# Kernel tuning notes

Hardware: AMD Instinct MI355X
Metric: run time of the kernel (lower is better)

The kernel has to match this reference:

```python
import jax, jax.numpy as jnp
import numpy as np

EPS = 1e-10
BETA_SCALE = 1.0
TEMP = 0.5


def setup_inputs() -> dict:
    key = jax.random.key(0)
    ks = jax.random.split(key, 8)
    D = 128
    return {
        "root_mu_min": jax.random.normal(ks[0], (1, 64, D), dtype=jnp.float32),
        "root_mu_max": jax.random.normal(ks[1], (1, 64, D), dtype=jnp.float32),
        "root_beta_min_raw": jax.random.normal(ks[2], (1, 64, D), dtype=jnp.float32),
        "root_beta_max_raw": jax.random.normal(ks[3], (1, 64, D), dtype=jnp.float32),
        "adj_logits0": jax.random.normal(ks[4], (512, 64), dtype=jnp.float32),
        "adj_logits1": jax.random.normal(ks[5], (2048, 512), dtype=jnp.float32),
        "u0": jax.random.uniform(ks[6], (1, 512, 64), dtype=jnp.float32),
        "u1": jax.random.uniform(ks[7], (1, 2048, 512), dtype=jnp.float32),
    }


def _gumbel_sigmoid_hard(logits, u):
    # gumbel noise from externally supplied uniforms, straight-through hard threshold
    g = -jnp.log(-jnp.log(u + EPS) + EPS)
    y_soft = jax.nn.sigmoid((logits + g) / TEMP)
    y_hard = (y_soft > 0.5).astype(y_soft.dtype)
    return y_hard - jax.lax.stop_gradient(y_soft) + y_soft


def _weighted_intersection(mu_min, mu_max, beta_min, beta_max, w):
    # w: (1, C, P); parent boxes: (1, P, D)
    wsum = jnp.sum(w, axis=2)[..., None] + EPS                      # (1, C, 1)
    b_min = jnp.einsum('bcp,bpd->bcd', w, beta_min) / wsum           # (1, C, D)
    b_max = jnp.einsum('bcp,bpd->bcd', w, beta_max) / wsum           # (1, C, D)
    logw = jnp.log(w + EPS)[..., None]                               # (1, C, P, 1)
    arg_min = logw + mu_min[:, None, :, :] / b_min[:, :, None, :]    # (1, C, P, D)
    mu_min_i = b_min * jax.nn.logsumexp(arg_min, axis=2)             # (1, C, D)
    arg_max = logw - mu_max[:, None, :, :] / b_max[:, :, None, :]    # (1, C, P, D)
    mu_max_i = -b_max * jax.nn.logsumexp(arg_max, axis=2)            # (1, C, D)
    return mu_min_i, mu_max_i, b_min, b_max


def reference(root_mu_min, root_mu_max, root_beta_min_raw, root_beta_max_raw,
              adj_logits0, adj_logits1, u0, u1):
    beta_min = jax.nn.sigmoid(root_beta_min_raw) * BETA_SCALE + 1e-6
    beta_max = jax.nn.sigmoid(root_beta_max_raw) * BETA_SCALE + 1e-6
    level = (root_mu_min, root_mu_max, beta_min, beta_max)
    outs = list(level)
    for logits, u in ((adj_logits0, u0), (adj_logits1, u1)):
        w = _gumbel_sigmoid_hard(logits[None], u)  # (1, C, P)
        level = _weighted_intersection(*level, w)
        outs.extend(level)
    return tuple(outs)
```

## Files before the change

kernel.cpp:

```cpp
#include <hip/hip_runtime.h>
#include <cmath>

#define DD 128
#define LOG2E 1.4426950408889634f

__device__ __forceinline__ float sigm(float x) { return 1.0f / (1.0f + __expf(-x)); }

__device__ __forceinline__ unsigned fenc(float f) {
    unsigned b = __float_as_uint(f);
    return (b & 0x80000000u) ? ~b : (b | 0x80000000u);
}
__device__ __forceinline__ float fdec(unsigned e) {
    return (e & 0x80000000u) ? __uint_as_float(e ^ 0x80000000u) : __uint_as_float(~e);
}

__global__ __launch_bounds__(512)
void k_root0(const float* __restrict__ mu_min, const float* __restrict__ mu_max,
             const float* __restrict__ braw_min, const float* __restrict__ braw_max,
             float* __restrict__ out,
             float2* __restrict__ mu2_0, float2* __restrict__ bb2_0,
             unsigned* __restrict__ e_min0, unsigned* __restrict__ e_neg0) {
    __shared__ float r1[4][DD], r2[4][DD];
    const int i = blockIdx.x * 512 + threadIdx.x;
    const int rg = threadIdx.x >> 7, d = threadIdx.x & (DD - 1);
    float mn = mu_min[i], mx = mu_max[i];
    float bm = sigm(braw_min[i]) + 1e-6f;
    float bx = sigm(braw_max[i]) + 1e-6f;
    out[i] = mn; out[8192 + i] = mx; out[16384 + i] = bm; out[24576 + i] = bx;
    mu2_0[i] = make_float2(mn, mx);
    bb2_0[i] = make_float2(bm, bx);
    r1[rg][d] = mn; r2[rg][d] = -mx;
    __syncthreads();
    if (threadIdx.x < DD) {
        float a = fmaxf(fmaxf(r1[0][d], r1[1][d]), fmaxf(r1[2][d], r1[3][d]));
        float b = fmaxf(fmaxf(r2[0][d], r2[1][d]), fmaxf(r2[2][d], r2[3][d]));
        atomicMax(e_min0 + d, fenc(a));
        atomicMax(e_neg0 + d, fenc(b));
        if (blockIdx.x == 0) {
            mu2_0[64 * DD + d] = make_float2(-1e38f, 1e38f);
            bb2_0[64 * DD + d] = make_float2(0.0f, 0.0f);
        }
    }
}

template<int P, int RPB>
__global__ __launch_bounds__(512)
void k_packprep(const float* __restrict__ mu_min, const float* __restrict__ mu_max,
                const float* __restrict__ b_min, const float* __restrict__ b_max,
                float2* __restrict__ mu2, float2* __restrict__ bb2,
                unsigned* __restrict__ e_min, unsigned* __restrict__ e_neg) {
    __shared__ float s1[4][DD], s2[4][DD];
    const int d = threadIdx.x & (DD - 1);
    const int rg = threadIdx.x >> 7;
    const int r0 = blockIdx.x * RPB;
    float m1 = -INFINITY, m2 = -INFINITY;
    for (int r = rg; r < RPB; r += 4) {
        int i = (r0 + r) * DD + d;
        float a = mu_min[i], b = mu_max[i];
        mu2[i] = make_float2(a, b);
        bb2[i] = make_float2(b_min[i], b_max[i]);
        m1 = fmaxf(m1, a);
        m2 = fmaxf(m2, -b);
    }
    s1[rg][d] = m1; s2[rg][d] = m2;
    __syncthreads();
    if (threadIdx.x < DD) {
        float a = fmaxf(fmaxf(s1[0][d], s1[1][d]), fmaxf(s1[2][d], s1[3][d]));
        float b = fmaxf(fmaxf(s2[0][d], s2[1][d]), fmaxf(s2[2][d], s2[3][d]));
        atomicMax(e_min + d, fenc(a));
        atomicMax(e_neg + d, fenc(b));
        if (blockIdx.x == 0) {
            mu2[P * DD + d] = make_float2(-1e38f, 1e38f);
            bb2[P * DD + d] = make_float2(0.0f, 0.0f);
        }
    }
}

template<int P>
__global__ __launch_bounds__(256, 4)
void k_levelw(const float* __restrict__ logits, const float* __restrict__ u,
              const float2* __restrict__ bb2, const float2* __restrict__ mu2,
              const unsigned* __restrict__ e_min, const unsigned* __restrict__ e_neg,
              float* __restrict__ o_mu_min, float* __restrict__ o_mu_max,
              float* __restrict__ o_b_min, float* __restrict__ o_b_max) {
    __shared__ __align__(16) int plist[2][P];
    __shared__ float4 red[2][2][64];
    const int tid = threadIdx.x;
    const int w = tid >> 6;
    const int lane = tid & 63;
    const int j = w >> 1, h = w & 1;
    const int c = blockIdx.x * 2 + j;
    int* pl = plist[j];

    int base = 0;
    #pragma unroll
    for (int it = 0; it < P / 64; ++it) {
        int p = it * 64 + lane;
        int idx = c * P + p;
        float uu = u[idx] + 1e-10f;
        float g = -__logf(-__logf(uu) + 1e-10f);
        bool pres = (logits[idx] + g) > 0.0f;
        unsigned long long m = __ballot(pres);
        if (pres) {
            int pos = __popcll(m & ((1ull << lane) - 1));
            pl[base + pos] = p << 10;
        }
        base += (int)__popcll(m);
    }
    const int n = base;
    int npad = (n + 15) & ~15;
    if (npad == 0) npad = 16;
    if (lane < npad - n) pl[n + lane] = P << 10;

    const unsigned lb = (unsigned)(lane << 4);
    const char* bbc = (const char*)bb2;
    const char* muc = (const char*)mu2;
    const int Th = npad >> 4;

    float dmn0 = 0.f, dmx0 = 0.f, dmn1 = 0.f, dmx1 = 0.f;
    {
        float4 q[8];
        int k = h * 8;
        {
            int4 A = *(const int4*)(pl + k);
            int4 B = *(const int4*)(pl + k + 4);
            q[0] = *(const float4*)(bbc + ((unsigned)A.x + lb));
            q[1] = *(const float4*)(bbc + ((unsigned)A.y + lb));
            q[2] = *(const float4*)(bbc + ((unsigned)A.z + lb));
            q[3] = *(const float4*)(bbc + ((unsigned)A.w + lb));
            q[4] = *(const float4*)(bbc + ((unsigned)B.x + lb));
            q[5] = *(const float4*)(bbc + ((unsigned)B.y + lb));
            q[6] = *(const float4*)(bbc + ((unsigned)B.z + lb));
            q[7] = *(const float4*)(bbc + ((unsigned)B.w + lb));
        }
        for (int t = 1; t < Th; ++t) {
            k += 16;
            int4 A = *(const int4*)(pl + k);
            int4 B = *(const int4*)(pl + k + 4);
            float4 qn[8];
            qn[0] = *(const float4*)(bbc + ((unsigned)A.x + lb));
            qn[1] = *(const float4*)(bbc + ((unsigned)A.y + lb));
            qn[2] = *(const float4*)(bbc + ((unsigned)A.z + lb));
            qn[3] = *(const float4*)(bbc + ((unsigned)A.w + lb));
            qn[4] = *(const float4*)(bbc + ((unsigned)B.x + lb));
            qn[5] = *(const float4*)(bbc + ((unsigned)B.y + lb));
            qn[6] = *(const float4*)(bbc + ((unsigned)B.z + lb));
            qn[7] = *(const float4*)(bbc + ((unsigned)B.w + lb));
            dmn0 += (q[0].x + q[1].x) + (q[2].x + q[3].x) + (q[4].x + q[5].x) + (q[6].x + q[7].x);
            dmx0 += (q[0].y + q[1].y) + (q[2].y + q[3].y) + (q[4].y + q[5].y) + (q[6].y + q[7].y);
            dmn1 += (q[0].z + q[1].z) + (q[2].z + q[3].z) + (q[4].z + q[5].z) + (q[6].z + q[7].z);
            dmx1 += (q[0].w + q[1].w) + (q[2].w + q[3].w) + (q[4].w + q[5].w) + (q[6].w + q[7].w);
            #pragma unroll
            for (int z = 0; z < 8; ++z) q[z] = qn[z];
        }
        dmn0 += (q[0].x + q[1].x) + (q[2].x + q[3].x) + (q[4].x + q[5].x) + (q[6].x + q[7].x);
        dmx0 += (q[0].y + q[1].y) + (q[2].y + q[3].y) + (q[4].y + q[5].y) + (q[6].y + q[7].y);
        dmn1 += (q[0].z + q[1].z) + (q[2].z + q[3].z) + (q[4].z + q[5].z) + (q[6].z + q[7].z);
        dmx1 += (q[0].w + q[1].w) + (q[2].w + q[3].w) + (q[4].w + q[5].w) + (q[6].w + q[7].w);
    }
    red[j][h][lane] = make_float4(dmn0, dmx0, dmn1, dmx1);
    __syncthreads();

    float4 pb0 = red[j][0][lane];
    float4 pb1 = red[j][1][lane];
    const float wsv = (float)n + 1e-10f;
    const float bmin0 = (pb0.x + pb1.x) / wsv;
    const float bmax0 = (pb0.y + pb1.y) / wsv;
    const float bmin1 = (pb0.z + pb1.z) / wsv;
    const float bmax1 = (pb0.w + pb1.w) / wsv;
    const float rmin0 = 1.0f / fmaxf(bmin0, 1e-30f);
    const float rmin1 = 1.0f / fmaxf(bmin1, 1e-30f);
    const float nrmax0 = -1.0f / fmaxf(bmax0, 1e-30f);
    const float nrmax1 = -1.0f / fmaxf(bmax1, 1e-30f);
    uint2 em = *(const uint2*)(e_min + 2 * lane);
    uint2 en = *(const uint2*)(e_neg + 2 * lane);
    const float Mm0 = fdec(em.x), Mm1 = fdec(em.y);
    const float Mg0 = fdec(en.x), Mg1 = fdec(en.y);
    const float rm20 = rmin0 * LOG2E, rm21 = rmin1 * LOG2E;
    const float nx20 = nrmax0 * LOG2E, nx21 = nrmax1 * LOG2E;
    const float nM10 = -rm20 * Mm0, nM11 = -rm21 * Mm1;
    const float nM20 = nx20 * Mg0, nM21 = nx21 * Mg1;
    __syncthreads();

    float s10 = 0.f, s20 = 0.f, s11 = 0.f, s21 = 0.f;
    {
        float4 q[8];
        int k = h * 8;
        {
            int4 A = *(const int4*)(pl + k);
            int4 B = *(const int4*)(pl + k + 4);
            q[0] = *(const float4*)(muc + ((unsigned)A.x + lb));
            q[1] = *(const float4*)(muc + ((unsigned)A.y + lb));
            q[2] = *(const float4*)(muc + ((unsigned)A.z + lb));
            q[3] = *(const float4*)(muc + ((unsigned)A.w + lb));
            q[4] = *(const float4*)(muc + ((unsigned)B.x + lb));
            q[5] = *(const float4*)(muc + ((unsigned)B.y + lb));
            q[6] = *(const float4*)(muc + ((unsigned)B.z + lb));
            q[7] = *(const float4*)(muc + ((unsigned)B.w + lb));
        }
        for (int t = 1; t < Th; ++t) {
            k += 16;
            int4 A = *(const int4*)(pl + k);
            int4 B = *(const int4*)(pl + k + 4);
            float4 qn[8];
            qn[0] = *(const float4*)(muc + ((unsigned)A.x + lb));
            qn[1] = *(const float4*)(muc + ((unsigned)A.y + lb));
            qn[2] = *(const float4*)(muc + ((unsigned)A.z + lb));
            qn[3] = *(const float4*)(muc + ((unsigned)A.w + lb));
            qn[4] = *(const float4*)(muc + ((unsigned)B.x + lb));
            qn[5] = *(const float4*)(muc + ((unsigned)B.y + lb));
            qn[6] = *(const float4*)(muc + ((unsigned)B.z + lb));
            qn[7] = *(const float4*)(muc + ((unsigned)B.w + lb));
            #pragma unroll
            for (int z = 0; z < 8; ++z) {
                s10 += __builtin_amdgcn_exp2f(fmaf(q[z].x, rm20, nM10));
                s20 += __builtin_amdgcn_exp2f(fmaf(q[z].y, nx20, nM20));
                s11 += __builtin_amdgcn_exp2f(fmaf(q[z].z, rm21, nM11));
                s21 += __builtin_amdgcn_exp2f(fmaf(q[z].w, nx21, nM21));
            }
            #pragma unroll
            for (int z = 0; z < 8; ++z) q[z] = qn[z];
        }
        #pragma unroll
        for (int z = 0; z < 8; ++z) {
            s10 += __builtin_amdgcn_exp2f(fmaf(q[z].x, rm20, nM10));
            s20 += __builtin_amdgcn_exp2f(fmaf(q[z].y, nx20, nM20));
            s11 += __builtin_amdgcn_exp2f(fmaf(q[z].z, rm21, nM11));
            s21 += __builtin_amdgcn_exp2f(fmaf(q[z].w, nx21, nM21));
        }
    }
    red[j][h][lane] = make_float4(s10, s20, s11, s21);
    __syncthreads();

    if (h == 0) {
        float4 pc0 = red[j][0][lane];
        float4 pc1 = red[j][1][lane];
        const float S10 = fmaxf(pc0.x + pc1.x, 1e-35f);
        const float S20 = fmaxf(pc0.y + pc1.y, 1e-35f);
        const float S11 = fmaxf(pc0.z + pc1.z, 1e-35f);
        const float S21 = fmaxf(pc0.w + pc1.w, 1e-35f);
        const int idx = c * DD + 2 * lane;
        float v10 = bmin0 * fmaf(rmin0, Mm0, __logf(S10));
        float v11 = bmin1 * fmaf(rmin1, Mm1, __logf(S11));
        float v20 = -bmax0 * fmaf(-nrmax0, Mg0, __logf(S20));
        float v21 = -bmax1 * fmaf(-nrmax1, Mg1, __logf(S21));
        *(float2*)(o_mu_min + idx) = make_float2(v10, v11);
        *(float2*)(o_mu_max + idx) = make_float2(v20, v21);
        *(float2*)(o_b_min + idx)  = make_float2(bmin0, bmin1);
        *(float2*)(o_b_max + idx)  = make_float2(bmax0, bmax1);
    }
}

extern "C" void kernel_launch(void* const* d_in, const int* in_sizes, int n_in,
                              void* d_out, int out_size, void* d_ws, size_t ws_size,
                              hipStream_t stream) {
    const float* mu_min0  = (const float*)d_in[0];
    const float* mu_max0  = (const float*)d_in[1];
    const float* braw_min = (const float*)d_in[2];
    const float* braw_max = (const float*)d_in[3];
    const float* adj0     = (const float*)d_in[4];
    const float* adj1     = (const float*)d_in[5];
    const float* u0       = (const float*)d_in[6];
    const float* u1       = (const float*)d_in[7];
    float* out = (float*)d_out;
    float* ws = (float*)d_ws;

    unsigned* cm_enc  = (unsigned*)ws;
    unsigned* cm0_min = cm_enc;
    unsigned* cm0_neg = cm_enc + 128;
    unsigned* cm1_min = cm_enc + 256;
    unsigned* cm1_neg = cm_enc + 384;
    float2* mu2_0 = (float2*)(ws + 512);
    float2* bb2_0 = mu2_0 + 65 * DD;
    float2* mu2_1 = bb2_0 + 65 * DD;
    float2* bb2_1 = mu2_1 + 513 * DD;


    hipMemsetAsync(cm_enc, 0, 512 * sizeof(unsigned), stream);

    k_root0<<<dim3(16), dim3(512), 0, stream>>>(
        mu_min0, mu_max0, braw_min, braw_max, out, mu2_0, bb2_0, cm0_min, cm0_neg);

    k_levelw<64><<<dim3(256), dim3(256), 0, stream>>>(
        adj0, u0, bb2_0, mu2_0, cm0_min, cm0_neg,
        out + 32768, out + 98304, out + 163840, out + 229376);

    k_packprep<512, 8><<<dim3(64), dim3(512), 0, stream>>>(
        out + 32768, out + 98304, out + 163840, out + 229376, mu2_1, bb2_1, cm1_min, cm1_neg);

    k_levelw<512><<<dim3(1024), dim3(256), 0, stream>>>(
        adj1, u1, bb2_1, mu2_1, cm1_min, cm1_neg,
        out + 294912, out + 557056, out + 819200, out + 1081344);
}
```

Baseline: 132.1 us.

## Replace sparse gather level-1 kernel with dense 4-child tiled weighted kernel

```diff
diff --git a/kernel.cpp b/kernel.cpp
--- a/kernel.cpp
+++ b/kernel.cpp
@@ -118,45 +118,22 @@
     const int Th = npad >> 4;
 
     float dmn0 = 0.f, dmx0 = 0.f, dmn1 = 0.f, dmx1 = 0.f;
-    {
-        float4 q[8];
-        int k = h * 8;
-        {
-            int4 A = *(const int4*)(pl + k);
-            int4 B = *(const int4*)(pl + k + 4);
-            q[0] = *(const float4*)(bbc + ((unsigned)A.x + lb));
-            q[1] = *(const float4*)(bbc + ((unsigned)A.y + lb));
-            q[2] = *(const float4*)(bbc + ((unsigned)A.z + lb));
-            q[3] = *(const float4*)(bbc + ((unsigned)A.w + lb));
-            q[4] = *(const float4*)(bbc + ((unsigned)B.x + lb));
-            q[5] = *(const float4*)(bbc + ((unsigned)B.y + lb));
-            q[6] = *(const float4*)(bbc + ((unsigned)B.z + lb));
-            q[7] = *(const float4*)(bbc + ((unsigned)B.w + lb));
-        }
-        for (int t = 1; t < Th; ++t) {
-            k += 16;
-            int4 A = *(const int4*)(pl + k);
-            int4 B = *(const int4*)(pl + k + 4);
-            float4 qn[8];
-            qn[0] = *(const float4*)(bbc + ((unsigned)A.x + lb));
-            qn[1] = *(const float4*)(bbc + ((unsigned)A.y + lb));
-            qn[2] = *(const float4*)(bbc + ((unsigned)A.z + lb));
-            qn[3] = *(const float4*)(bbc + ((unsigned)A.w + lb));
-            qn[4] = *(const float4*)(bbc + ((unsigned)B.x + lb));
-            qn[5] = *(const float4*)(bbc + ((unsigned)B.y + lb));
-            qn[6] = *(const float4*)(bbc + ((unsigned)B.z + lb));
-            qn[7] = *(const float4*)(bbc + ((unsigned)B.w + lb));
-            dmn0 += (q[0].x + q[1].x) + (q[2].x + q[3].x) + (q[4].x + q[5].x) + (q[6].x + q[7].x);
-            dmx0 += (q[0].y + q[1].y) + (q[2].y + q[3].y) + (q[4].y + q[5].y) + (q[6].y + q[7].y);
-            dmn1 += (q[0].z + q[1].z) + (q[2].z + q[3].z) + (q[4].z + q[5].z) + (q[6].z + q[7].z);
-            dmx1 += (q[0].w + q[1].w) + (q[2].w + q[3].w) + (q[4].w + q[5].w) + (q[6].w + q[7].w);
-            #pragma unroll
-            for (int z = 0; z < 8; ++z) q[z] = qn[z];
-        }
-        dmn0 += (q[0].x + q[1].x) + (q[2].x + q[3].x) + (q[4].x + q[5].x) + (q[6].x + q[7].x);
-        dmx0 += (q[0].y + q[1].y) + (q[2].y + q[3].y) + (q[4].y + q[5].y) + (q[6].y + q[7].y);
-        dmn1 += (q[0].z + q[1].z) + (q[2].z + q[3].z) + (q[4].z + q[5].z) + (q[6].z + q[7].z);
-        dmx1 += (q[0].w + q[1].w) + (q[2].w + q[3].w) + (q[4].w + q[5].w) + (q[6].w + q[7].w);
+    for (int t = 0; t < Th; ++t) {
+        int k = h * 8 + t * 16;
+        int4 A = *(const int4*)(pl + k);
+        int4 B = *(const int4*)(pl + k + 4);
+        float4 q0 = *(const float4*)(bbc + ((unsigned)A.x + lb));
+        float4 q1 = *(const float4*)(bbc + ((unsigned)A.y + lb));
+        float4 q2 = *(const float4*)(bbc + ((unsigned)A.z + lb));
+        float4 q3 = *(const float4*)(bbc + ((unsigned)A.w + lb));
+        float4 q4 = *(const float4*)(bbc + ((unsigned)B.x + lb));
+        float4 q5 = *(const float4*)(bbc + ((unsigned)B.y + lb));
+        float4 q6 = *(const float4*)(bbc + ((unsigned)B.z + lb));
+        float4 q7 = *(const float4*)(bbc + ((unsigned)B.w + lb));
+        dmn0 += (q0.x + q1.x) + (q2.x + q3.x) + (q4.x + q5.x) + (q6.x + q7.x);
+        dmx0 += (q0.y + q1.y) + (q2.y + q3.y) + (q4.y + q5.y) + (q6.y + q7.y);
+        dmn1 += (q0.z + q1.z) + (q2.z + q3.z) + (q4.z + q5.z) + (q6.z + q7.z);
+        dmx1 += (q0.w + q1.w) + (q2.w + q3.w) + (q4.w + q5.w) + (q6.w + q7.w);
     }
     red[j][h][lane] = make_float4(dmn0, dmx0, dmn1, dmx1);
     __syncthreads();
@@ -183,51 +160,50 @@
     __syncthreads();
 
     float s10 = 0.f, s20 = 0.f, s11 = 0.f, s21 = 0.f;
-    {
-        float4 q[8];
-        int k = h * 8;
-        {
-            int4 A = *(const int4*)(pl + k);
-            int4 B = *(const int4*)(pl + k + 4);
-            q[0] = *(const float4*)(muc + ((unsigned)A.x + lb));
-            q[1] = *(const float4*)(muc + ((unsigned)A.y + lb));
-            q[2] = *(const float4*)(muc + ((unsigned)A.z + lb));
-            q[3] = *(const float4*)(muc + ((unsigned)A.w + lb));
-            q[4] = *(const float4*)(muc + ((unsigned)B.x + lb));
-            q[5] = *(const float4*)(muc + ((unsigned)B.y + lb));
-            q[6] = *(const float4*)(muc + ((unsigned)B.z + lb));
-            q[7] = *(const float4*)(muc + ((unsigned)B.w + lb));
-        }
-        for (int t = 1; t < Th; ++t) {
-            k += 16;
-            int4 A = *(const int4*)(pl + k);
-            int4 B = *(const int4*)(pl + k + 4);
-            float4 qn[8];
-            qn[0] = *(const float4*)(muc + ((unsigned)A.x + lb));
-            qn[1] = *(const float4*)(muc + ((unsigned)A.y + lb));
-            qn[2] = *(const float4*)(muc + ((unsigned)A.z + lb));
-            qn[3] = *(const float4*)(muc + ((unsigned)A.w + lb));
-            qn[4] = *(const float4*)(muc + ((unsigned)B.x + lb));
-            qn[5] = *(const float4*)(muc + ((unsigned)B.y + lb));
-            qn[6] = *(const float4*)(muc + ((unsigned)B.z + lb));
-            qn[7] = *(const float4*)(muc + ((unsigned)B.w + lb));
-            #pragma unroll
-            for (int z = 0; z < 8; ++z) {
-                s10 += __builtin_amdgcn_exp2f(fmaf(q[z].x, rm20, nM10));
-                s20 += __builtin_amdgcn_exp2f(fmaf(q[z].y, nx20, nM20));
-                s11 += __builtin_amdgcn_exp2f(fmaf(q[z].z, rm21, nM11));
-                s21 += __builtin_amdgcn_exp2f(fmaf(q[z].w, nx21, nM21));
-            }
-            #pragma unroll
-            for (int z = 0; z < 8; ++z) q[z] = qn[z];
-        }
-        #pragma unroll
-        for (int z = 0; z < 8; ++z) {
-            s10 += __builtin_amdgcn_exp2f(fmaf(q[z].x, rm20, nM10));
-            s20 += __builtin_amdgcn_exp2f(fmaf(q[z].y, nx20, nM20));
-            s11 += __builtin_amdgcn_exp2f(fmaf(q[z].z, rm21, nM11));
-            s21 += __builtin_amdgcn_exp2f(fmaf(q[z].w, nx21, nM21));
-        }
+    for (int t = 0; t < Th; ++t) {
+        int k = h * 8 + t * 16;
+        int4 A = *(const int4*)(pl + k);
+        int4 B = *(const int4*)(pl + k + 4);
+        float4 q0 = *(const float4*)(muc + ((unsigned)A.x + lb));
+        float4 q1 = *(const float4*)(muc + ((unsigned)A.y + lb));
+        float4 q2 = *(const float4*)(muc + ((unsigned)A.z + lb));
+        float4 q3 = *(const float4*)(muc + ((unsigned)A.w + lb));
+        float4 q4 = *(const float4*)(muc + ((unsigned)B.x + lb));
+        float4 q5 = *(const float4*)(muc + ((unsigned)B.y + lb));
+        float4 q6 = *(const float4*)(muc + ((unsigned)B.z + lb));
+        float4 q7 = *(const float4*)(muc + ((unsigned)B.w + lb));
+        s10 += __builtin_amdgcn_exp2f(fmaf(q0.x, rm20, nM10));
+        s20 += __builtin_amdgcn_exp2f(fmaf(q0.y, nx20, nM20));
+        s11 += __builtin_amdgcn_exp2f(fmaf(q0.z, rm21, nM11));
+        s21 += __builtin_amdgcn_exp2f(fmaf(q0.w, nx21, nM21));
+        s10 += __builtin_amdgcn_exp2f(fmaf(q1.x, rm20, nM10));
+        s20 += __builtin_amdgcn_exp2f(fmaf(q1.y, nx20, nM20));
+        s11 += __builtin_amdgcn_exp2f(fmaf(q1.z, rm21, nM11));
+        s21 += __builtin_amdgcn_exp2f(fmaf(q1.w, nx21, nM21));
+        s10 += __builtin_amdgcn_exp2f(fmaf(q2.x, rm20, nM10));
+        s20 += __builtin_amdgcn_exp2f(fmaf(q2.y, nx20, nM20));
+        s11 += __builtin_amdgcn_exp2f(fmaf(q2.z, rm21, nM11));
+        s21 += __builtin_amdgcn_exp2f(fmaf(q2.w, nx21, nM21));
+        s10 += __builtin_amdgcn_exp2f(fmaf(q3.x, rm20, nM10));
+        s20 += __builtin_amdgcn_exp2f(fmaf(q3.y, nx20, nM20));
+        s11 += __builtin_amdgcn_exp2f(fmaf(q3.z, rm21, nM11));
+        s21 += __builtin_amdgcn_exp2f(fmaf(q3.w, nx21, nM21));
+        s10 += __builtin_amdgcn_exp2f(fmaf(q4.x, rm20, nM10));
+        s20 += __builtin_amdgcn_exp2f(fmaf(q4.y, nx20, nM20));
+        s11 += __builtin_amdgcn_exp2f(fmaf(q4.z, rm21, nM11));
+        s21 += __builtin_amdgcn_exp2f(fmaf(q4.w, nx21, nM21));
+        s10 += __builtin_amdgcn_exp2f(fmaf(q5.x, rm20, nM10));
+        s20 += __builtin_amdgcn_exp2f(fmaf(q5.y, nx20, nM20));
+        s11 += __builtin_amdgcn_exp2f(fmaf(q5.z, rm21, nM11));
+        s21 += __builtin_amdgcn_exp2f(fmaf(q5.w, nx21, nM21));
+        s10 += __builtin_amdgcn_exp2f(fmaf(q6.x, rm20, nM10));
+        s20 += __builtin_amdgcn_exp2f(fmaf(q6.y, nx20, nM20));
+        s11 += __builtin_amdgcn_exp2f(fmaf(q6.z, rm21, nM11));
+        s21 += __builtin_amdgcn_exp2f(fmaf(q6.w, nx21, nM21));
+        s10 += __builtin_amdgcn_exp2f(fmaf(q7.x, rm20, nM10));
+        s20 += __builtin_amdgcn_exp2f(fmaf(q7.y, nx20, nM20));
+        s11 += __builtin_amdgcn_exp2f(fmaf(q7.z, rm21, nM11));
+        s21 += __builtin_amdgcn_exp2f(fmaf(q7.w, nx21, nM21));
     }
     red[j][h][lane] = make_float4(s10, s20, s11, s21);
     __syncthreads();
@@ -251,6 +227,151 @@
     }
 }
 
+__global__ __launch_bounds__(512, 4)
+void k_level2d(const float* __restrict__ logits, const float* __restrict__ u,
+               const float2* __restrict__ bb2, const float2* __restrict__ mu2,
+               const unsigned* __restrict__ e_min, const unsigned* __restrict__ e_neg,
+               float* __restrict__ o_mu_min, float* __restrict__ o_mu_max,
+               float* __restrict__ o_b_min, float* __restrict__ o_b_max) {
+    constexpr int P = 512, TC = 4;
+    __shared__ __align__(16) float wsh[P][TC];
+    __shared__ int npres[TC];
+    __shared__ float4 red[8][TC][64];
+    __shared__ float4 carrA[TC][64], carrB[TC][64];
+    const int tid = threadIdx.x;
+    const int w = tid >> 6;
+    const int lane = tid & 63;
+    const int c0 = blockIdx.x * TC;
+    if (tid < TC) npres[tid] = 0;
+    __syncthreads();
+
+    #pragma unroll
+    for (int it = 0; it < TC; ++it) {
+        int i = it * 512 + tid;
+        int j = i >> 9;
+        int p = i & 511;
+        int idx = (c0 + j) * P + p;
+        float uu = u[idx] + 1e-10f;
+        float g = -__logf(-__logf(uu) + 1e-10f);
+        bool pres = (logits[idx] + g) > 0.0f;
+        wsh[p][j] = pres ? 1.0f : 1e-10f;
+        unsigned long long m = __ballot(pres);
+        if (lane == 0) atomicAdd(&npres[j], (int)__popcll(m));
+    }
+    __syncthreads();
+
+    const unsigned lb = (unsigned)(lane << 4);
+    const char* bbc = (const char*)bb2 + (unsigned)(w * 64) * 1024u + lb;
+    const char* muc = (const char*)mu2 + (unsigned)(w * 64) * 1024u + lb;
+    const int p0 = w * 64;
+
+    float4 accB[TC];
+    #pragma unroll
+    for (int j = 0; j < TC; ++j) accB[j] = make_float4(0.f, 0.f, 0.f, 0.f);
+    for (int z = 0; z < 64; z += 4) {
+        float4 q0 = *(const float4*)(bbc + (unsigned)(z + 0) * 1024u);
+        float4 q1 = *(const float4*)(bbc + (unsigned)(z + 1) * 1024u);
+        float4 q2 = *(const float4*)(bbc + (unsigned)(z + 2) * 1024u);
+        float4 q3 = *(const float4*)(bbc + (unsigned)(z + 3) * 1024u);
+        float4 w0 = *(const float4*)wsh[p0 + z + 0];
+        float4 w1 = *(const float4*)wsh[p0 + z + 1];
+        float4 w2 = *(const float4*)wsh[p0 + z + 2];
+        float4 w3 = *(const float4*)wsh[p0 + z + 3];
+        const float* wf0 = (const float*)&w0;
+        const float* wf1 = (const float*)&w1;
+        const float* wf2 = (const float*)&w2;
+        const float* wf3 = (const float*)&w3;
+        #pragma unroll
+        for (int j = 0; j < TC; ++j) {
+            accB[j].x = fmaf(wf0[j], q0.x, fmaf(wf1[j], q1.x, fmaf(wf2[j], q2.x, fmaf(wf3[j], q3.x, accB[j].x))));
+            accB[j].y = fmaf(wf0[j], q0.y, fmaf(wf1[j], q1.y, fmaf(wf2[j], q2.y, fmaf(wf3[j], q3.y, accB[j].y))));
+            accB[j].z = fmaf(wf0[j], q0.z, fmaf(wf1[j], q1.z, fmaf(wf2[j], q2.z, fmaf(wf3[j], q3.z, accB[j].z))));
+            accB[j].w = fmaf(wf0[j], q0.w, fmaf(wf1[j], q1.w, fmaf(wf2[j], q2.w, fmaf(wf3[j], q3.w, accB[j].w))));
+        }
+    }
+    #pragma unroll
+    for (int j = 0; j < TC; ++j) red[w][j][lane] = accB[j];
+    __syncthreads();
+
+    float bmin0, bmax0, bmin1, bmax1, rmin0, rmin1, nrmax0, nrmax1, Mm0, Mm1, Mg0, Mg1;
+    const int rj = tid >> 6;
+    if (tid < 256) {
+        float4 S = red[0][rj][lane];
+        #pragma unroll
+        for (int ww = 1; ww < 8; ++ww) {
+            float4 t = red[ww][rj][lane];
+            S.x += t.x; S.y += t.y; S.z += t.z; S.w += t.w;
+        }
+        const float wsv = (float)npres[rj] + 1e-10f;
+        bmin0 = S.x / wsv; bmax0 = S.y / wsv; bmin1 = S.z / wsv; bmax1 = S.w / wsv;
+        rmin0 = 1.0f / fmaxf(bmin0, 1e-30f);
+        rmin1 = 1.0f / fmaxf(bmin1, 1e-30f);
+        nrmax0 = -1.0f / fmaxf(bmax0, 1e-30f);
+        nrmax1 = -1.0f / fmaxf(bmax1, 1e-30f);
+        uint2 em = *(const uint2*)(e_min + 2 * lane);
+        uint2 en = *(const uint2*)(e_neg + 2 * lane);
+        Mm0 = fdec(em.x); Mm1 = fdec(em.y);
+        Mg0 = fdec(en.x); Mg1 = fdec(en.y);
+        float rm20 = rmin0 * LOG2E, rm21 = rmin1 * LOG2E;
+        float nx20 = nrmax0 * LOG2E, nx21 = nrmax1 * LOG2E;
+        carrA[rj][lane] = make_float4(rm20, rm21, nx20, nx21);
+        carrB[rj][lane] = make_float4(-rm20 * Mm0, -rm21 * Mm1, nx20 * Mg0, nx21 * Mg1);
+    }
+    __syncthreads();
+
+    float4 cA[TC], cB[TC];
+    #pragma unroll
+    for (int j = 0; j < TC; ++j) { cA[j] = carrA[j][lane]; cB[j] = carrB[j][lane]; }
+
+    float4 accS[TC];
+    #pragma unroll
+    for (int j = 0; j < TC; ++j) accS[j] = make_float4(0.f, 0.f, 0.f, 0.f);
+    for (int z = 0; z < 64; z += 2) {
+        float4 q0 = *(const float4*)(muc + (unsigned)(z + 0) * 1024u);
+        float4 q1 = *(const float4*)(muc + (unsigned)(z + 1) * 1024u);
+        float4 w0 = *(const float4*)wsh[p0 + z + 0];
+        float4 w1 = *(const float4*)wsh[p0 + z + 1];
+        const float* wf0 = (const float*)&w0;
+        const float* wf1 = (const float*)&w1;
+        #pragma unroll
+        for (int j = 0; j < TC; ++j) {
+            accS[j].x = fmaf(wf0[j], __builtin_amdgcn_exp2f(fmaf(q0.x, cA[j].x, cB[j].x)), accS[j].x);
+            accS[j].y = fmaf(wf0[j], __builtin_amdgcn_exp2f(fmaf(q0.y, cA[j].z, cB[j].z)), accS[j].y);
+            accS[j].z = fmaf(wf0[j], __builtin_amdgcn_exp2f(fmaf(q0.z, cA[j].y, cB[j].y)), accS[j].z);
+            accS[j].w = fmaf(wf0[j], __builtin_amdgcn_exp2f(fmaf(q0.w, cA[j].w, cB[j].w)), accS[j].w);
+            accS[j].x = fmaf(wf1[j], __builtin_amdgcn_exp2f(fmaf(q1.x, cA[j].x, cB[j].x)), accS[j].x);
+            accS[j].y = fmaf(wf1[j], __builtin_amdgcn_exp2f(fmaf(q1.y, cA[j].z, cB[j].z)), accS[j].y);
+            accS[j].z = fmaf(wf1[j], __builtin_amdgcn_exp2f(fmaf(q1.z, cA[j].y, cB[j].y)), accS[j].z);
+            accS[j].w = fmaf(wf1[j], __builtin_amdgcn_exp2f(fmaf(q1.w, cA[j].w, cB[j].w)), accS[j].w);
+        }
+    }
+    #pragma unroll
+    for (int j = 0; j < TC; ++j) red[w][j][lane] = accS[j];
+    __syncthreads();
+
+    if (tid < 256) {
+        float4 S = red[0][rj][lane];
+        #pragma unroll
+        for (int ww = 1; ww < 8; ++ww) {
+            float4 t = red[ww][rj][lane];
+            S.x += t.x; S.y += t.y; S.z += t.z; S.w += t.w;
+        }
+        const float S10 = fmaxf(S.x, 1e-35f);
+        const float S20 = fmaxf(S.y, 1e-35f);
+        const float S11 = fmaxf(S.z, 1e-35f);
+        const float S21 = fmaxf(S.w, 1e-35f);
+        const int idx = (c0 + rj) * DD + 2 * lane;
+        float v10 = bmin0 * fmaf(rmin0, Mm0, __logf(S10));
+        float v11 = bmin1 * fmaf(rmin1, Mm1, __logf(S11));
+        float v20 = -bmax0 * fmaf(-nrmax0, Mg0, __logf(S20));
+        float v21 = -bmax1 * fmaf(-nrmax1, Mg1, __logf(S21));
+        *(float2*)(o_mu_min + idx) = make_float2(v10, v11);
+        *(float2*)(o_mu_max + idx) = make_float2(v20, v21);
+        *(float2*)(o_b_min + idx)  = make_float2(bmin0, bmin1);
+        *(float2*)(o_b_max + idx)  = make_float2(bmax0, bmax1);
+    }
+}
+
 extern "C" void kernel_launch(void* const* d_in, const int* in_sizes, int n_in,
                               void* d_out, int out_size, void* d_ws, size_t ws_size,
                               hipStream_t stream) {
@@ -288,7 +409,7 @@
     k_packprep<512, 8><<<dim3(64), dim3(512), 0, stream>>>(
         out + 32768, out + 98304, out + 163840, out + 229376, mu2_1, bb2_1, cm1_min, cm1_neg);
 
-    k_levelw<512><<<dim3(1024), dim3(256), 0, stream>>>(
+    k_level2d<<<dim3(512), dim3(512), 0, stream>>>(
         adj1, u1, bb2_1, mu2_1, cm1_min, cm1_neg,
         out + 294912, out + 557056, out + 819200, out + 1081344);
 }
```

New measurement: 125.4 us. 5.0% less time.
